# Kernel tuning notes

Hardware: AMD Instinct MI355X
Metric: run time of the kernel (lower is better)

## Reference

```python
import jax, jax.numpy as jnp
import numpy as np

WIN = (7, 7)      # window_size
SHIFT = (3, 3)    # shift_size
NUM_HEADS = 8
DIM = 256


def _relative_position_index(wh, ww):
    # static int index table, computed with numpy (constant under jit)
    coords = np.stack(np.meshgrid(np.arange(wh), np.arange(ww), indexing='ij'))  # [2,wh,ww]
    flat = coords.reshape(2, -1)                                                  # [2,N]
    rel = flat[:, :, None] - flat[:, None, :]                                     # [2,N,N]
    rel = rel.transpose(1, 2, 0).copy()
    rel[:, :, 0] += wh - 1
    rel[:, :, 1] += ww - 1
    rel[:, :, 0] *= 2 * ww - 1
    return rel.sum(-1).reshape(-1)  # [N*N]


def _attn_mask(pad_h, pad_w, win, shift):
    # static shifted-window region mask, numpy constants
    mask = np.zeros((pad_h, pad_w), dtype=np.float32)
    h_slices = ((0, -win[0]), (-win[0], -shift[0]), (-shift[0], None))
    w_slices = ((0, -win[1]), (-win[1], -shift[1]), (-shift[1], None))
    cnt = 0
    for h0, h1 in h_slices:
        for w0, w1 in w_slices:
            mask[h0:h1, w0:w1] = cnt
            cnt += 1
    nwh, nww = pad_h // win[0], pad_w // win[1]
    mask = mask.reshape(nwh, win[0], nww, win[1]).transpose(0, 2, 1, 3).reshape(nwh * nww, win[0] * win[1])
    diff = mask[:, None, :] - mask[:, :, None]
    return np.where(diff != 0, -100.0, 0.0).astype(np.float32)  # [nW, N, N]


def shifted_window_attention(x, qkv_weight, qkv_bias, proj_weight, proj_bias, rel_pos_table):
    B, H, W, C = x.shape
    wh, ww = WIN
    pad_b = (wh - H % wh) % wh
    pad_r = (ww - W % ww) % ww
    x = jnp.pad(x, ((0, 0), (0, pad_b), (0, pad_r), (0, 0)))
    pad_h, pad_w = H + pad_b, W + pad_r
    # replicate the original's shift-disable logic exactly
    sw, sh = SHIFT[0], SHIFT[1]
    if wh >= pad_h:
        sh = 0
    if ww >= pad_w:
        sw = 0
    shift = (sw, sh)
    shifted = sum(shift) > 0
    if shifted:
        x = jnp.roll(x, shift=(-shift[0], -shift[1]), axis=(1, 2))

    nwh, nww = pad_h // wh, pad_w // ww
    nW = nwh * nww
    N = wh * ww
    # window partition: [B*nW, N, C]
    xw = x.reshape(B, nwh, wh, nww, ww, C).transpose(0, 1, 3, 2, 4, 5).reshape(B * nW, N, C)

    qkv = xw @ qkv_weight.T + qkv_bias  # [B*nW, N, 3C]
    hd = C // NUM_HEADS
    qkv = qkv.reshape(B * nW, N, 3, NUM_HEADS, hd).transpose(2, 0, 3, 1, 4)  # [3, B*nW, H, N, hd]
    q, k, v = qkv[0], qkv[1], qkv[2]

    scale = hd ** (-0.5)
    attn = jnp.einsum('bhnd,bhmd->bhnm', q * scale, k)  # [B*nW, H, N, N]

    # relative position bias
    idx = _relative_position_index(wh, ww)  # static [N*N]
    bias = rel_pos_table[idx].reshape(N, N, NUM_HEADS).transpose(2, 0, 1)[None]  # [1,H,N,N]
    attn = attn + bias

    if shifted:
        mask = jnp.asarray(_attn_mask(pad_h, pad_w, WIN, shift))  # [nW, N, N]
        attn = attn.reshape(B, nW, NUM_HEADS, N, N) + mask[None, :, None, :, :]
        attn = attn.reshape(B * nW, NUM_HEADS, N, N)

    attn = jax.nn.softmax(attn, axis=-1)
    out = jnp.einsum('bhnm,bhmd->bhnd', attn, v)  # [B*nW, H, N, hd]
    out = out.transpose(0, 2, 1, 3).reshape(B * nW, N, C)
    out = out @ proj_weight.T + proj_bias

    # reverse window partition
    out = out.reshape(B, nwh, nww, wh, ww, C).transpose(0, 1, 3, 2, 4, 5).reshape(B, pad_h, pad_w, C)
    if shifted:
        out = jnp.roll(out, shift=(shift[0], shift[1]), axis=(1, 2))
    return out[:, :H, :W, :]


def setup_inputs() -> dict:
    key = jax.random.key(0)
    ks = jax.random.split(key, 6)
    return {
        'x': jax.random.normal(ks[0], (32, 56, 56, DIM), dtype=jnp.float32),
        'qkv_weight': jax.random.normal(ks[1], (3 * DIM, DIM), dtype=jnp.float32) * 0.02,
        'qkv_bias': jax.random.normal(ks[2], (3 * DIM,), dtype=jnp.float32) * 0.02,
        'proj_weight': jax.random.normal(ks[3], (DIM, DIM), dtype=jnp.float32) * 0.02,
        'proj_bias': jax.random.normal(ks[4], (DIM,), dtype=jnp.float32) * 0.02,
        'rel_pos_table': jax.random.normal(ks[5], ((2 * WIN[0] - 1) * (2 * WIN[1] - 1), NUM_HEADS), dtype=jnp.float32) * 0.02,
    }


def reference(x, qkv_weight, qkv_bias, proj_weight, proj_bias, rel_pos_table):
    return shifted_window_attention(x, qkv_weight, qkv_bias, proj_weight, proj_bias, rel_pos_table)
```

## Files before the change

### kernel.cpp

```cpp
#include <hip/hip_runtime.h>
#include <stdint.h>

typedef __attribute__((ext_vector_type(4))) float f32x4;
typedef __attribute__((ext_vector_type(8))) short bf16x8;
typedef __attribute__((ext_vector_type(8))) unsigned short u16x8;
typedef __attribute__((ext_vector_type(4))) unsigned short u16x4;

#define NPIX 100352
#define CDIM 256
#define QKVN 768
#define HWDIM 56

__device__ __forceinline__ unsigned short f2bf(float f) {
  union { float f; unsigned int u; } cv; cv.f = f;
  unsigned int u = cv.u;
  unsigned int r = (u + 0x7FFFu + ((u >> 16) & 1u)) >> 16;
  return (unsigned short)r;
}
__device__ __forceinline__ float bf2f(unsigned short h) {
  union { unsigned int u; float f; } cv; cv.u = ((unsigned int)h) << 16;
  return cv.f;
}

__global__ __launch_bounds__(256) void wqkv_pre(const float* __restrict__ w,
                                                unsigned short* __restrict__ wtab) {
  int e8 = blockIdx.x * 256 + threadIdx.x;
  int l = e8 & 63;
  int t1 = e8 >> 6;
  int wsel = t1 & 1;
  int ks = (t1 >> 1) & 7;
  int h = (t1 >> 4) & 7;
  int m = t1 >> 7;
  int row = m * 256 + h * 32 + wsel * 16 + (l & 15);
  int col = ks * 32 + (l >> 4) * 8;
  const float4* src = reinterpret_cast<const float4*>(w + (size_t)row * 256 + col);
  float4 a = src[0], b = src[1];
  u16x8 r;
  r[0] = f2bf(a.x); r[1] = f2bf(a.y); r[2] = f2bf(a.z); r[3] = f2bf(a.w);
  r[4] = f2bf(b.x); r[5] = f2bf(b.y); r[6] = f2bf(b.z); r[7] = f2bf(b.w);
  *reinterpret_cast<u16x8*>(wtab + (size_t)e8 * 8) = r;
}

__global__ __launch_bounds__(256) void wproj_pre(const float* __restrict__ w,
                                                 unsigned short* __restrict__ wptab) {
  int e8 = blockIdx.x * 256 + threadIdx.x;
  int l = e8 & 63;
  int t1 = e8 >> 6;
  int wsel = t1 & 1;
  int ks = (t1 >> 1) & 7;
  int h = (t1 >> 4) & 7;
  int row = h * 32 + wsel * 16 + (l & 15);
  int col = ks * 32 + (l >> 4) * 8;
  const float4* src = reinterpret_cast<const float4*>(w + (size_t)row * 256 + col);
  float4 a = src[0], b = src[1];
  u16x8 r;
  r[0] = f2bf(a.x); r[1] = f2bf(a.y); r[2] = f2bf(a.z); r[3] = f2bf(a.w);
  r[4] = f2bf(b.x); r[5] = f2bf(b.y); r[6] = f2bf(b.z); r[7] = f2bf(b.w);
  *reinterpret_cast<u16x8*>(wptab + (size_t)e8 * 8) = r;
}

__global__ __launch_bounds__(256) void bias_pre(const float* __restrict__ table,
                                                unsigned short* __restrict__ bt) {
  int e = blockIdx.x * 256 + threadIdx.x;
  int r  = e & 3;
  int fr = (e >> 2) & 15;
  int q  = (e >> 6) & 3;
  int c2 = (e >> 8) & 3;
  int jf = (e >> 10) & 3;
  int h  = (e >> 12) & 7;
  int cls = (e >> 15) & 3;
  int j = jf * 16 + q * 4 + r;
  int i = c2 * 16 + fr;
  float v;
  if (j > 48 || i > 48) {
    v = -1e30f;
  } else {
    int bh = cls >> 1, bw = cls & 1;
    int iwi = i / 7, iwj = i % 7;
    int jwi = j / 7, jwj = j % 7;
    int ireg = (bh ? ((iwi < 4) ? 1 : 2) : 0) * 3 + (bw ? ((iwj < 4) ? 1 : 2) : 0);
    int jreg = (bh ? ((jwi < 4) ? 1 : 2) : 0) * 3 + (bw ? ((jwj < 4) ? 1 : 2) : 0);
    float m = (ireg == jreg) ? 0.f : -100.f;
    v = table[((iwi - jwi + 6) * 13 + (iwj - jwj + 6)) * 8 + h] + m;
  }
  bt[e] = f2bf(v);
}

__global__ __launch_bounds__(512, 2) void fused_attn(
    const float* __restrict__ x,
    const unsigned short* __restrict__ wtab,
    const float* __restrict__ bqkv,
    const unsigned short* __restrict__ btab,
    const unsigned short* __restrict__ wptab,
    const float* __restrict__ bproj,
    float* __restrict__ out)
{
  const int win = blockIdx.x;
  const int b = win >> 6;
  const int gi = (win >> 3) & 7;
  const int gj = win & 7;
  const int t = threadIdx.x;
  const int head = t >> 6;
  const int lane = t & 63;
  const int fr = lane & 15;
  const int q = lane >> 4;

  __shared__ unsigned short x_s[49 * 256];
  __shared__ unsigned short Vt[8][32 * 70];
  __shared__ int pix_s[64];

  if (t < 64) {
    int idx = (t < 49) ? t : 48;
    int wi = idx / 7, wj = idx - (idx / 7) * 7;
    int hs = gi * 7 + wi, ws2 = gj * 7 + wj;
    int ph = hs + 3; if (ph >= HWDIM) ph -= HWDIM;
    int pw = ws2 + 3; if (pw >= HWDIM) pw -= HWDIM;
    pix_s[t] = (b * HWDIM + ph) * HWDIM + pw;
  }
  __syncthreads();

  #define XS(row, bc) ((unsigned)((row) * 512 + (((bc)) ^ (((row) & 7) << 4))))

  for (int u = t; u < 49 * 32; u += 512) {
    int pix = u >> 5, seg = u & 31;
    const float4* src = reinterpret_cast<const float4*>(x + (size_t)pix_s[pix] * CDIM + seg * 8);
    float4 a = src[0], c = src[1];
    u16x8 r;
    r[0] = f2bf(a.x); r[1] = f2bf(a.y); r[2] = f2bf(a.z); r[3] = f2bf(a.w);
    r[4] = f2bf(c.x); r[5] = f2bf(c.y); r[6] = f2bf(c.z); r[7] = f2bf(c.w);
    *reinterpret_cast<u16x8*>((char*)x_s + XS(pix, seg * 16)) = r;
  }
  __syncthreads();

  const int cls = (((gi == 7) ? 1 : 0) << 1) | ((gj == 7) ? 1 : 0);
  const unsigned short* bth = btab + (((cls << 3) | head) << 12);
  unsigned short* VtW = Vt[head];
  const int srcA = ((q & 1) << 5) + fr;
  const int srcB = srcA + 16;
  const bool hi = (q >= 2);

  #define PACK_MAT(pkm)                                                                \
  { _Pragma("unroll") for (int d = 0; d < 2; ++d)                                      \
      _Pragma("unroll") for (int p2 = 0; p2 < 4; ++p2) {                               \
        pkm[d][p2][0] = (unsigned)f2bf(acc[d][p2][0]) | ((unsigned)f2bf(acc[d][p2][1]) << 16); \
        pkm[d][p2][1] = (unsigned)f2bf(acc[d][p2][2]) | ((unsigned)f2bf(acc[d][p2][3]) << 16); \
      } }

  #define BUILD_FRAG(pkm, p2, dst)                                                     \
  { unsigned a0 = (unsigned)__shfl((int)pkm[0][p2][0], srcA);                          \
    unsigned a1 = (unsigned)__shfl((int)pkm[0][p2][1], srcA);                          \
    unsigned a2 = (unsigned)__shfl((int)pkm[0][p2][0], srcB);                          \
    unsigned a3 = (unsigned)__shfl((int)pkm[0][p2][1], srcB);                          \
    unsigned b0 = (unsigned)__shfl((int)pkm[1][p2][0], srcA);                          \
    unsigned b1 = (unsigned)__shfl((int)pkm[1][p2][1], srcA);                          \
    unsigned b2 = (unsigned)__shfl((int)pkm[1][p2][0], srcB);                          \
    unsigned b3 = (unsigned)__shfl((int)pkm[1][p2][1], srcB);                          \
    union { unsigned u[4]; bf16x8 v; } uf;                                             \
    uf.u[0] = hi ? b0 : a0; uf.u[1] = hi ? b1 : a1;                                    \
    uf.u[2] = hi ? b2 : a2; uf.u[3] = hi ? b3 : a3;                                    \
    dst = uf.v; }

  unsigned pkk[2][4][2], pkq[2][4][2];
  {
    f32x4 acc[2][4];
    #pragma unroll 1
    for (int m = 0; m < 3; ++m) {
      const int mat = 2 - m;
      #pragma unroll
      for (int d = 0; d < 2; ++d)
        #pragma unroll
        for (int p2 = 0; p2 < 4; ++p2)
          acc[d][p2] = (f32x4){0.f, 0.f, 0.f, 0.f};
      #pragma unroll
      for (int ks = 0; ks < 8; ++ks) {
        const unsigned short* wb = wtab + (size_t)((((mat * 8 + head) * 8 + ks) * 128 + lane) * 8);
        bf16x8 wf0 = *reinterpret_cast<const bf16x8*>(wb);
        bf16x8 wf1 = *reinterpret_cast<const bf16x8*>(wb + 512);
        int bc = ks * 64 + q * 16;
        bf16x8 xf0 = *reinterpret_cast<const bf16x8*>((const char*)x_s + XS(fr, bc));
        bf16x8 xf1 = *reinterpret_cast<const bf16x8*>((const char*)x_s + XS(16 + fr, bc));
        bf16x8 xf2 = *reinterpret_cast<const bf16x8*>((const char*)x_s + XS(32 + fr, bc));
        bf16x8 x3r = *reinterpret_cast<const bf16x8*>((const char*)x_s + XS(48, bc));
        bf16x8 xf3 = (fr == 0) ? x3r : (bf16x8){0, 0, 0, 0, 0, 0, 0, 0};
        acc[0][0] = __builtin_amdgcn_mfma_f32_16x16x32_bf16(wf0, xf0, acc[0][0], 0, 0, 0);
        acc[0][1] = __builtin_amdgcn_mfma_f32_16x16x32_bf16(wf0, xf1, acc[0][1], 0, 0, 0);
        acc[0][2] = __builtin_amdgcn_mfma_f32_16x16x32_bf16(wf0, xf2, acc[0][2], 0, 0, 0);
        acc[0][3] = __builtin_amdgcn_mfma_f32_16x16x32_bf16(wf0, xf3, acc[0][3], 0, 0, 0);
        acc[1][0] = __builtin_amdgcn_mfma_f32_16x16x32_bf16(wf1, xf0, acc[1][0], 0, 0, 0);
        acc[1][1] = __builtin_amdgcn_mfma_f32_16x16x32_bf16(wf1, xf1, acc[1][1], 0, 0, 0);
        acc[1][2] = __builtin_amdgcn_mfma_f32_16x16x32_bf16(wf1, xf2, acc[1][2], 0, 0, 0);
        acc[1][3] = __builtin_amdgcn_mfma_f32_16x16x32_bf16(wf1, xf3, acc[1][3], 0, 0, 0);
      }
      #pragma unroll
      for (int d = 0; d < 2; ++d) {
        f32x4 bv = *reinterpret_cast<const f32x4*>(bqkv + mat * 256 + head * 32 + d * 16 + q * 4);
        acc[d][0] += bv; acc[d][1] += bv; acc[d][2] += bv; acc[d][3] += bv;
      }
      if (mat == 2) {
        #pragma unroll
        for (int d = 0; d < 2; ++d)
          #pragma unroll
          for (int p2 = 0; p2 < 4; ++p2)
            #pragma unroll
            for (int r = 0; r < 4; ++r)
              VtW[(d * 16 + q * 4 + r) * 70 + p2 * 16 + fr] = f2bf(acc[d][p2][r]);
      } else if (mat == 1) {
        PACK_MAT(pkk);
      } else {
        PACK_MAT(pkq);
      }
    }
  }

  bf16x8 qf[4];
  BUILD_FRAG(pkq, 0, qf[0]); BUILD_FRAG(pkq, 1, qf[1]);
  BUILD_FRAG(pkq, 2, qf[2]); BUILD_FRAG(pkq, 3, qf[3]);

  const float scale = 0.17677669529663687f;
  u16x4 aw[2][4];
  #pragma unroll
  for (int c2 = 0; c2 < 4; ++c2)
    aw[0][c2] = *reinterpret_cast<const u16x4*>(bth + (c2 << 8) + (q << 6) + (fr << 2));
  float colsum[4] = {0.f, 0.f, 0.f, 0.f};
  unsigned pk[4][4][2];
  #pragma unroll
  for (int jf = 0; jf < 4; ++jf) {
    bf16x8 kfj;
    BUILD_FRAG(pkk, jf, kfj);
    f32x4 sacc[4];
    #pragma unroll
    for (int c2 = 0; c2 < 4; ++c2) {
      f32x4 z = {0.f, 0.f, 0.f, 0.f};
      sacc[c2] = __builtin_amdgcn_mfma_f32_16x16x32_bf16(kfj, qf[c2], z, 0, 0, 0);
    }
    if (jf < 3) {
      #pragma unroll
      for (int c2 = 0; c2 < 4; ++c2)
        aw[(jf + 1) & 1][c2] = *reinterpret_cast<const u16x4*>(
            bth + (((jf + 1) * 4 + c2) << 8) + (q << 6) + (fr << 2));
    }
    #pragma unroll
    for (int c2 = 0; c2 < 4; ++c2) {
      float ev[4];
      #pragma unroll
      for (int r = 0; r < 4; ++r) {
        float val = fmaf(sacc[c2][r], scale, bf2f(aw[jf & 1][c2][r]));
        ev[r] = __expf(val);
        colsum[c2] += ev[r];
      }
      unsigned h0 = f2bf(ev[0]), h1 = f2bf(ev[1]);
      unsigned h2 = f2bf(ev[2]), h3 = f2bf(ev[3]);
      pk[jf][c2][0] = h0 | (h1 << 16);
      pk[jf][c2][1] = h2 | (h3 << 16);
    }
  }
  float rinv[4];
  #pragma unroll
  for (int c2 = 0; c2 < 4; ++c2) {
    float s = colsum[c2];
    s += __shfl_xor(s, 16);
    s += __shfl_xor(s, 32);
    rinv[c2] = 1.0f / s;
  }

  f32x4 outT[2][4] = {};
  #pragma unroll
  for (int kb = 0; kb < 2; ++kb) {
    bf16x8 vf0 = *reinterpret_cast<const bf16x8*>(&VtW[(fr)      * 70 + kb * 32 + q * 8]);
    bf16x8 vf1 = *reinterpret_cast<const bf16x8*>(&VtW[(16 + fr) * 70 + kb * 32 + q * 8]);
    #pragma unroll
    for (int c2 = 0; c2 < 4; ++c2) {
      bf16x8 pf;
      {
        unsigned a0 = (unsigned)__shfl((int)pk[2 * kb][c2][0], srcA);
        unsigned a1 = (unsigned)__shfl((int)pk[2 * kb][c2][1], srcA);
        unsigned a2 = (unsigned)__shfl((int)pk[2 * kb][c2][0], srcB);
        unsigned a3 = (unsigned)__shfl((int)pk[2 * kb][c2][1], srcB);
        unsigned b0 = (unsigned)__shfl((int)pk[2 * kb + 1][c2][0], srcA);
        unsigned b1 = (unsigned)__shfl((int)pk[2 * kb + 1][c2][1], srcA);
        unsigned b2 = (unsigned)__shfl((int)pk[2 * kb + 1][c2][0], srcB);
        unsigned b3 = (unsigned)__shfl((int)pk[2 * kb + 1][c2][1], srcB);
        union { unsigned u[4]; bf16x8 v; } pfv;
        pfv.u[0] = hi ? b0 : a0;
        pfv.u[1] = hi ? b1 : a1;
        pfv.u[2] = hi ? b2 : a2;
        pfv.u[3] = hi ? b3 : a3;
        pf = pfv.v;
      }
      outT[0][c2] = __builtin_amdgcn_mfma_f32_16x16x32_bf16(vf0, pf, outT[0][c2], 0, 0, 0);
      outT[1][c2] = __builtin_amdgcn_mfma_f32_16x16x32_bf16(vf1, pf, outT[1][c2], 0, 0, 0);
    }
  }

  unsigned short* out_s = x_s;
  __syncthreads();
  #pragma unroll
  for (int c2 = 0; c2 < 4; ++c2) {
    int i = c2 * 16 + fr;
    if (i < 49) {
      float rv = rinv[c2];
      #pragma unroll
      for (int nt = 0; nt < 2; ++nt) {
        f32x4 o = outT[nt][c2];
        u16x4 pkd;
        pkd[0] = f2bf(o[0] * rv); pkd[1] = f2bf(o[1] * rv);
        pkd[2] = f2bf(o[2] * rv); pkd[3] = f2bf(o[3] * rv);
        *reinterpret_cast<u16x4*>((char*)out_s + XS(i, head * 64 + nt * 32 + q * 8)) = pkd;
      }
    }
  }
  __syncthreads();

  {
    f32x4 pacc[2][4];
    #pragma unroll
    for (int w = 0; w < 2; ++w)
      #pragma unroll
      for (int p2 = 0; p2 < 4; ++p2)
        pacc[w][p2] = (f32x4){0.f, 0.f, 0.f, 0.f};
    #pragma unroll
    for (int ks = 0; ks < 8; ++ks) {
      const unsigned short* wb = wptab + (size_t)((((head * 8 + ks) * 2) * 64 + lane) * 8);
      bf16x8 wp0 = *reinterpret_cast<const bf16x8*>(wb);
      bf16x8 wp1 = *reinterpret_cast<const bf16x8*>(wb + 512);
      int bc = ks * 64 + q * 16;
      bf16x8 of0 = *reinterpret_cast<const bf16x8*>((const char*)out_s + XS(fr, bc));
      bf16x8 of1 = *reinterpret_cast<const bf16x8*>((const char*)out_s + XS(16 + fr, bc));
      bf16x8 of2 = *reinterpret_cast<const bf16x8*>((const char*)out_s + XS(32 + fr, bc));
      bf16x8 o3r = *reinterpret_cast<const bf16x8*>((const char*)out_s + XS(48, bc));
      bf16x8 of3 = (fr == 0) ? o3r : (bf16x8){0, 0, 0, 0, 0, 0, 0, 0};
      pacc[0][0] = __builtin_amdgcn_mfma_f32_16x16x32_bf16(of0, wp0, pacc[0][0], 0, 0, 0);
      pacc[0][1] = __builtin_amdgcn_mfma_f32_16x16x32_bf16(of1, wp0, pacc[0][1], 0, 0, 0);
      pacc[0][2] = __builtin_amdgcn_mfma_f32_16x16x32_bf16(of2, wp0, pacc[0][2], 0, 0, 0);
      pacc[0][3] = __builtin_amdgcn_mfma_f32_16x16x32_bf16(of3, wp0, pacc[0][3], 0, 0, 0);
      pacc[1][0] = __builtin_amdgcn_mfma_f32_16x16x32_bf16(of0, wp1, pacc[1][0], 0, 0, 0);
      pacc[1][1] = __builtin_amdgcn_mfma_f32_16x16x32_bf16(of1, wp1, pacc[1][1], 0, 0, 0);
      pacc[1][2] = __builtin_amdgcn_mfma_f32_16x16x32_bf16(of2, wp1, pacc[1][2], 0, 0, 0);
      pacc[1][3] = __builtin_amdgcn_mfma_f32_16x16x32_bf16(of3, wp1, pacc[1][3], 0, 0, 0);
    }
    float bb0 = bproj[head * 32 + fr];
    float bb1 = bproj[head * 32 + 16 + fr];
    #pragma unroll
    for (int p2 = 0; p2 < 4; ++p2) {
      #pragma unroll
      for (int r = 0; r < 4; ++r) {
        int pix = p2 * 16 + q * 4 + r;
        if (pix < 49) {
          float* op = out + (size_t)pix_s[pix] * CDIM + head * 32 + fr;
          op[0]  = pacc[0][p2][r] + bb0;
          op[16] = pacc[1][p2][r] + bb1;
        }
      }
    }
  }
  #undef PACK_MAT
  #undef BUILD_FRAG
  #undef XS
}

extern "C" void kernel_launch(void* const* d_in, const int* in_sizes, int n_in,
                              void* d_out, int out_size, void* d_ws, size_t ws_size,
                              hipStream_t stream) {
  const float* x      = (const float*)d_in[0];
  const float* qkv_w  = (const float*)d_in[1];
  const float* qkv_b  = (const float*)d_in[2];
  const float* proj_w = (const float*)d_in[3];
  const float* proj_b = (const float*)d_in[4];
  const float* table  = (const float*)d_in[5];

  char* ws = (char*)d_ws;
  unsigned short* btab  = (unsigned short*)ws;
  unsigned short* wtab  = (unsigned short*)(ws + 262144);
  unsigned short* wptab = (unsigned short*)(ws + 655360);

  bias_pre<<<512, 256, 0, stream>>>(table, btab);
  wqkv_pre<<<96, 256, 0, stream>>>(qkv_w, wtab);
  wproj_pre<<<32, 256, 0, stream>>>(proj_w, wptab);

  fused_attn<<<2048, 512, 0, stream>>>(x, wtab, qkv_b, btab, wptab, proj_b,
                                       (float*)d_out);
}
```

Before: 157.3 us.

## Process four windows per persistent block and use packed bf16 conversion

Each block now loops over four consecutive windows instead of handling one, so the grid shrinks from 2048 to 512 blocks. The x-gather loop is unrolled with pixel addresses computed inline, which removes the barrier that used to follow the pix_s setup. Manual bf16 rounding is replaced with the packed __float22bfloat162_rn intrinsic. The aim is to amortise block launch and setup and to cut conversion instructions. In exchange there is an extra barrier per window and no overlap between windows inside a block, and 512 blocks at two per CU may leave CUs idle or the last wave unbalanced.

```diff
diff --git a/kernel.cpp b/kernel.cpp
--- a/kernel.cpp
+++ b/kernel.cpp
@@ -1,4 +1,5 @@
 #include <hip/hip_runtime.h>
+#include <hip/hip_bf16.h>
 #include <stdint.h>
 
 typedef __attribute__((ext_vector_type(4))) float f32x4;
@@ -20,6 +21,12 @@
 __device__ __forceinline__ float bf2f(unsigned short h) {
   union { unsigned int u; float f; } cv; cv.u = ((unsigned int)h) << 16;
   return cv.f;
+}
+__device__ __forceinline__ unsigned pk2(float lo, float hi) {
+  float2 a; a.x = lo; a.y = hi;
+  __hip_bfloat162 h = __float22bfloat162_rn(a);
+  union { __hip_bfloat162 h; unsigned u; } cv; cv.h = h;
+  return cv.u;
 }
 
 __global__ __launch_bounds__(256) void wqkv_pre(const float* __restrict__ w,
@@ -95,55 +102,30 @@
     const float* __restrict__ bproj,
     float* __restrict__ out)
 {
-  const int win = blockIdx.x;
-  const int b = win >> 6;
-  const int gi = (win >> 3) & 7;
-  const int gj = win & 7;
+  const int bid = blockIdx.x;
   const int t = threadIdx.x;
   const int head = t >> 6;
   const int lane = t & 63;
   const int fr = lane & 15;
   const int q = lane >> 4;
+  const int b = bid >> 4;
 
   __shared__ unsigned short x_s[49 * 256];
   __shared__ unsigned short Vt[8][32 * 70];
   __shared__ int pix_s[64];
 
-  if (t < 64) {
-    int idx = (t < 49) ? t : 48;
-    int wi = idx / 7, wj = idx - (idx / 7) * 7;
-    int hs = gi * 7 + wi, ws2 = gj * 7 + wj;
-    int ph = hs + 3; if (ph >= HWDIM) ph -= HWDIM;
-    int pw = ws2 + 3; if (pw >= HWDIM) pw -= HWDIM;
-    pix_s[t] = (b * HWDIM + ph) * HWDIM + pw;
-  }
-  __syncthreads();
-
-  #define XS(row, bc) ((unsigned)((row) * 512 + (((bc)) ^ (((row) & 7) << 4))))
-
-  for (int u = t; u < 49 * 32; u += 512) {
-    int pix = u >> 5, seg = u & 31;
-    const float4* src = reinterpret_cast<const float4*>(x + (size_t)pix_s[pix] * CDIM + seg * 8);
-    float4 a = src[0], c = src[1];
-    u16x8 r;
-    r[0] = f2bf(a.x); r[1] = f2bf(a.y); r[2] = f2bf(a.z); r[3] = f2bf(a.w);
-    r[4] = f2bf(c.x); r[5] = f2bf(c.y); r[6] = f2bf(c.z); r[7] = f2bf(c.w);
-    *reinterpret_cast<u16x8*>((char*)x_s + XS(pix, seg * 16)) = r;
-  }
-  __syncthreads();
-
-  const int cls = (((gi == 7) ? 1 : 0) << 1) | ((gj == 7) ? 1 : 0);
-  const unsigned short* bth = btab + (((cls << 3) | head) << 12);
-  unsigned short* VtW = Vt[head];
   const int srcA = ((q & 1) << 5) + fr;
   const int srcB = srcA + 16;
   const bool hi = (q >= 2);
+  unsigned short* VtW = Vt[head];
+
+  #define XS(row, bc) ((unsigned)((row) * 512 + (((bc)) ^ (((row) & 7) << 4))))
 
   #define PACK_MAT(pkm)                                                                \
   { _Pragma("unroll") for (int d = 0; d < 2; ++d)                                      \
       _Pragma("unroll") for (int p2 = 0; p2 < 4; ++p2) {                               \
-        pkm[d][p2][0] = (unsigned)f2bf(acc[d][p2][0]) | ((unsigned)f2bf(acc[d][p2][1]) << 16); \
-        pkm[d][p2][1] = (unsigned)f2bf(acc[d][p2][2]) | ((unsigned)f2bf(acc[d][p2][3]) << 16); \
+        pkm[d][p2][0] = pk2(acc[d][p2][0], acc[d][p2][1]);                             \
+        pkm[d][p2][1] = pk2(acc[d][p2][2], acc[d][p2][3]);                             \
       } }
 
   #define BUILD_FRAG(pkm, p2, dst)                                                     \
@@ -160,195 +142,232 @@
     uf.u[2] = hi ? b2 : a2; uf.u[3] = hi ? b3 : a3;                                    \
     dst = uf.v; }
 
-  unsigned pkk[2][4][2], pkq[2][4][2];
-  {
-    f32x4 acc[2][4];
-    #pragma unroll 1
-    for (int m = 0; m < 3; ++m) {
-      const int mat = 2 - m;
-      #pragma unroll
-      for (int d = 0; d < 2; ++d)
-        #pragma unroll
-        for (int p2 = 0; p2 < 4; ++p2)
-          acc[d][p2] = (f32x4){0.f, 0.f, 0.f, 0.f};
-      #pragma unroll
-      for (int ks = 0; ks < 8; ++ks) {
-        const unsigned short* wb = wtab + (size_t)((((mat * 8 + head) * 8 + ks) * 128 + lane) * 8);
-        bf16x8 wf0 = *reinterpret_cast<const bf16x8*>(wb);
-        bf16x8 wf1 = *reinterpret_cast<const bf16x8*>(wb + 512);
-        int bc = ks * 64 + q * 16;
-        bf16x8 xf0 = *reinterpret_cast<const bf16x8*>((const char*)x_s + XS(fr, bc));
-        bf16x8 xf1 = *reinterpret_cast<const bf16x8*>((const char*)x_s + XS(16 + fr, bc));
-        bf16x8 xf2 = *reinterpret_cast<const bf16x8*>((const char*)x_s + XS(32 + fr, bc));
-        bf16x8 x3r = *reinterpret_cast<const bf16x8*>((const char*)x_s + XS(48, bc));
-        bf16x8 xf3 = (fr == 0) ? x3r : (bf16x8){0, 0, 0, 0, 0, 0, 0, 0};
-        acc[0][0] = __builtin_amdgcn_mfma_f32_16x16x32_bf16(wf0, xf0, acc[0][0], 0, 0, 0);
-        acc[0][1] = __builtin_amdgcn_mfma_f32_16x16x32_bf16(wf0, xf1, acc[0][1], 0, 0, 0);
-        acc[0][2] = __builtin_amdgcn_mfma_f32_16x16x32_bf16(wf0, xf2, acc[0][2], 0, 0, 0);
-        acc[0][3] = __builtin_amdgcn_mfma_f32_16x16x32_bf16(wf0, xf3, acc[0][3], 0, 0, 0);
-        acc[1][0] = __builtin_amdgcn_mfma_f32_16x16x32_bf16(wf1, xf0, acc[1][0], 0, 0, 0);
-        acc[1][1] = __builtin_amdgcn_mfma_f32_16x16x32_bf16(wf1, xf1, acc[1][1], 0, 0, 0);
-        acc[1][2] = __builtin_amdgcn_mfma_f32_16x16x32_bf16(wf1, xf2, acc[1][2], 0, 0, 0);
-        acc[1][3] = __builtin_amdgcn_mfma_f32_16x16x32_bf16(wf1, xf3, acc[1][3], 0, 0, 0);
-      }
-      #pragma unroll
-      for (int d = 0; d < 2; ++d) {
-        f32x4 bv = *reinterpret_cast<const f32x4*>(bqkv + mat * 256 + head * 32 + d * 16 + q * 4);
-        acc[d][0] += bv; acc[d][1] += bv; acc[d][2] += bv; acc[d][3] += bv;
-      }
-      if (mat == 2) {
+  #pragma unroll 1
+  for (int g = 0; g < 4; ++g) {
+    const int win = (bid << 2) | g;
+    const int gi = (win >> 3) & 7;
+    const int gj = win & 7;
+
+    if (g) __syncthreads();
+
+    if (t < 64) {
+      int idx = (t < 49) ? t : 48;
+      int wi = idx / 7, wj = idx - (idx / 7) * 7;
+      int ph = gi * 7 + wi + 3; if (ph >= HWDIM) ph -= HWDIM;
+      int pw = gj * 7 + wj + 3; if (pw >= HWDIM) pw -= HWDIM;
+      pix_s[t] = (b * HWDIM + ph) * HWDIM + pw;
+    }
+
+    #pragma unroll
+    for (int k = 0; k < 4; ++k) {
+      int u = t + 512 * k;
+      if (u < 1568) {
+        int pix = u >> 5, seg = u & 31;
+        int wi = pix / 7, wj = pix - (pix / 7) * 7;
+        int ph = gi * 7 + wi + 3; if (ph >= HWDIM) ph -= HWDIM;
+        int pw = gj * 7 + wj + 3; if (pw >= HWDIM) pw -= HWDIM;
+        int pabs = (b * HWDIM + ph) * HWDIM + pw;
+        const float4* src = reinterpret_cast<const float4*>(x + (size_t)pabs * CDIM + seg * 8);
+        float4 a = src[0], c = src[1];
+        union { unsigned w[4]; u16x8 v; } r;
+        r.w[0] = pk2(a.x, a.y); r.w[1] = pk2(a.z, a.w);
+        r.w[2] = pk2(c.x, c.y); r.w[3] = pk2(c.z, c.w);
+        *reinterpret_cast<u16x8*>((char*)x_s + XS(pix, seg * 16)) = r.v;
+      }
+    }
+    __syncthreads();
+
+    const int cls = (((gi == 7) ? 1 : 0) << 1) | ((gj == 7) ? 1 : 0);
+    const unsigned short* bth = btab + (((cls << 3) | head) << 12);
+
+    unsigned pkk[2][4][2], pkq[2][4][2];
+    {
+      f32x4 acc[2][4];
+      #pragma unroll 1
+      for (int m = 0; m < 3; ++m) {
+        const int mat = 2 - m;
         #pragma unroll
         for (int d = 0; d < 2; ++d)
           #pragma unroll
           for (int p2 = 0; p2 < 4; ++p2)
+            acc[d][p2] = (f32x4){0.f, 0.f, 0.f, 0.f};
+        #pragma unroll
+        for (int ks = 0; ks < 8; ++ks) {
+          const unsigned short* wb = wtab + (size_t)((((mat * 8 + head) * 8 + ks) * 128 + lane) * 8);
+          bf16x8 wf0 = *reinterpret_cast<const bf16x8*>(wb);
+          bf16x8 wf1 = *reinterpret_cast<const bf16x8*>(wb + 512);
+          int bc = ks * 64 + q * 16;
+          bf16x8 xf0 = *reinterpret_cast<const bf16x8*>((const char*)x_s + XS(fr, bc));
+          bf16x8 xf1 = *reinterpret_cast<const bf16x8*>((const char*)x_s + XS(16 + fr, bc));
+          bf16x8 xf2 = *reinterpret_cast<const bf16x8*>((const char*)x_s + XS(32 + fr, bc));
+          bf16x8 x3r = *reinterpret_cast<const bf16x8*>((const char*)x_s + XS(48, bc));
+          bf16x8 xf3 = (fr == 0) ? x3r : (bf16x8){0, 0, 0, 0, 0, 0, 0, 0};
+          acc[0][0] = __builtin_amdgcn_mfma_f32_16x16x32_bf16(wf0, xf0, acc[0][0], 0, 0, 0);
+          acc[0][1] = __builtin_amdgcn_mfma_f32_16x16x32_bf16(wf0, xf1, acc[0][1], 0, 0, 0);
+          acc[0][2] = __builtin_amdgcn_mfma_f32_16x16x32_bf16(wf0, xf2, acc[0][2], 0, 0, 0);
+          acc[0][3] = __builtin_amdgcn_mfma_f32_16x16x32_bf16(wf0, xf3, acc[0][3], 0, 0, 0);
+          acc[1][0] = __builtin_amdgcn_mfma_f32_16x16x32_bf16(wf1, xf0, acc[1][0], 0, 0, 0);
+          acc[1][1] = __builtin_amdgcn_mfma_f32_16x16x32_bf16(wf1, xf1, acc[1][1], 0, 0, 0);
+          acc[1][2] = __builtin_amdgcn_mfma_f32_16x16x32_bf16(wf1, xf2, acc[1][2], 0, 0, 0);
+          acc[1][3] = __builtin_amdgcn_mfma_f32_16x16x32_bf16(wf1, xf3, acc[1][3], 0, 0, 0);
+        }
+        #pragma unroll
+        for (int d = 0; d < 2; ++d) {
+          f32x4 bv = *reinterpret_cast<const f32x4*>(bqkv + mat * 256 + head * 32 + d * 16 + q * 4);
+          acc[d][0] += bv; acc[d][1] += bv; acc[d][2] += bv; acc[d][3] += bv;
+        }
+        if (mat == 2) {
+          #pragma unroll
+          for (int d = 0; d < 2; ++d)
             #pragma unroll
-            for (int r = 0; r < 4; ++r)
-              VtW[(d * 16 + q * 4 + r) * 70 + p2 * 16 + fr] = f2bf(acc[d][p2][r]);
-      } else if (mat == 1) {
-        PACK_MAT(pkk);
-      } else {
-        PACK_MAT(pkq);
-      }
-    }
-  }
-
-  bf16x8 qf[4];
-  BUILD_FRAG(pkq, 0, qf[0]); BUILD_FRAG(pkq, 1, qf[1]);
-  BUILD_FRAG(pkq, 2, qf[2]); BUILD_FRAG(pkq, 3, qf[3]);
-
-  const float scale = 0.17677669529663687f;
-  u16x4 aw[2][4];
-  #pragma unroll
-  for (int c2 = 0; c2 < 4; ++c2)
-    aw[0][c2] = *reinterpret_cast<const u16x4*>(bth + (c2 << 8) + (q << 6) + (fr << 2));
-  float colsum[4] = {0.f, 0.f, 0.f, 0.f};
-  unsigned pk[4][4][2];
-  #pragma unroll
-  for (int jf = 0; jf < 4; ++jf) {
-    bf16x8 kfj;
-    BUILD_FRAG(pkk, jf, kfj);
-    f32x4 sacc[4];
+            for (int p2 = 0; p2 < 4; ++p2)
+              #pragma unroll
+              for (int r = 0; r < 4; ++r)
+                VtW[(d * 16 + q * 4 + r) * 70 + p2 * 16 + fr] = f2bf(acc[d][p2][r]);
+        } else if (mat == 1) {
+          PACK_MAT(pkk);
+        } else {
+          PACK_MAT(pkq);
+        }
+      }
+    }
+
+    bf16x8 qf[4];
+    BUILD_FRAG(pkq, 0, qf[0]); BUILD_FRAG(pkq, 1, qf[1]);
+    BUILD_FRAG(pkq, 2, qf[2]); BUILD_FRAG(pkq, 3, qf[3]);
+
+    const float scale = 0.17677669529663687f;
+    u16x4 aw[2][4];
+    #pragma unroll
+    for (int c2 = 0; c2 < 4; ++c2)
+      aw[0][c2] = *reinterpret_cast<const u16x4*>(bth + (c2 << 8) + (q << 6) + (fr << 2));
+    float colsum[4] = {0.f, 0.f, 0.f, 0.f};
+    unsigned pk[4][4][2];
+    #pragma unroll
+    for (int jf = 0; jf < 4; ++jf) {
+      bf16x8 kfj;
+      BUILD_FRAG(pkk, jf, kfj);
+      f32x4 sacc[4];
+      #pragma unroll
+      for (int c2 = 0; c2 < 4; ++c2) {
+        f32x4 z = {0.f, 0.f, 0.f, 0.f};
+        sacc[c2] = __builtin_amdgcn_mfma_f32_16x16x32_bf16(kfj, qf[c2], z, 0, 0, 0);
+      }
+      if (jf < 3) {
+        #pragma unroll
+        for (int c2 = 0; c2 < 4; ++c2)
+          aw[(jf + 1) & 1][c2] = *reinterpret_cast<const u16x4*>(
+              bth + (((jf + 1) * 4 + c2) << 8) + (q << 6) + (fr << 2));
+      }
+      #pragma unroll
+      for (int c2 = 0; c2 < 4; ++c2) {
+        float ev[4];
+        #pragma unroll
+        for (int r = 0; r < 4; ++r) {
+          float val = fmaf(sacc[c2][r], scale, bf2f(aw[jf & 1][c2][r]));
+          ev[r] = __expf(val);
+          colsum[c2] += ev[r];
+        }
+        pk[jf][c2][0] = pk2(ev[0], ev[1]);
+        pk[jf][c2][1] = pk2(ev[2], ev[3]);
+      }
+    }
+    float rinv[4];
     #pragma unroll
     for (int c2 = 0; c2 < 4; ++c2) {
-      f32x4 z = {0.f, 0.f, 0.f, 0.f};
-      sacc[c2] = __builtin_amdgcn_mfma_f32_16x16x32_bf16(kfj, qf[c2], z, 0, 0, 0);
-    }
-    if (jf < 3) {
-      #pragma unroll
-      for (int c2 = 0; c2 < 4; ++c2)
-        aw[(jf + 1) & 1][c2] = *reinterpret_cast<const u16x4*>(
-            bth + (((jf + 1) * 4 + c2) << 8) + (q << 6) + (fr << 2));
-    }
+      float s = colsum[c2];
+      s += __shfl_xor(s, 16);
+      s += __shfl_xor(s, 32);
+      rinv[c2] = 1.0f / s;
+    }
+
+    f32x4 outT[2][4] = {};
+    #pragma unroll
+    for (int kb = 0; kb < 2; ++kb) {
+      bf16x8 vf0 = *reinterpret_cast<const bf16x8*>(&VtW[(fr)      * 70 + kb * 32 + q * 8]);
+      bf16x8 vf1 = *reinterpret_cast<const bf16x8*>(&VtW[(16 + fr) * 70 + kb * 32 + q * 8]);
+      #pragma unroll
+      for (int c2 = 0; c2 < 4; ++c2) {
+        bf16x8 pf;
+        {
+          unsigned a0 = (unsigned)__shfl((int)pk[2 * kb][c2][0], srcA);
+          unsigned a1 = (unsigned)__shfl((int)pk[2 * kb][c2][1], srcA);
+          unsigned a2 = (unsigned)__shfl((int)pk[2 * kb][c2][0], srcB);
+          unsigned a3 = (unsigned)__shfl((int)pk[2 * kb][c2][1], srcB);
+          unsigned b0 = (unsigned)__shfl((int)pk[2 * kb + 1][c2][0], srcA);
+          unsigned b1 = (unsigned)__shfl((int)pk[2 * kb + 1][c2][1], srcA);
+          unsigned b2 = (unsigned)__shfl((int)pk[2 * kb + 1][c2][0], srcB);
+          unsigned b3 = (unsigned)__shfl((int)pk[2 * kb + 1][c2][1], srcB);
+          union { unsigned u[4]; bf16x8 v; } pfv;
+          pfv.u[0] = hi ? b0 : a0;
+          pfv.u[1] = hi ? b1 : a1;
+          pfv.u[2] = hi ? b2 : a2;
+          pfv.u[3] = hi ? b3 : a3;
+          pf = pfv.v;
+        }
+        outT[0][c2] = __builtin_amdgcn_mfma_f32_16x16x32_bf16(vf0, pf, outT[0][c2], 0, 0, 0);
+        outT[1][c2] = __builtin_amdgcn_mfma_f32_16x16x32_bf16(vf1, pf, outT[1][c2], 0, 0, 0);
+      }
+    }
+
+    unsigned short* out_s = x_s;
+    __syncthreads();
     #pragma unroll
     for (int c2 = 0; c2 < 4; ++c2) {
-      float ev[4];
-      #pragma unroll
-      for (int r = 0; r < 4; ++r) {
-        float val = fmaf(sacc[c2][r], scale, bf2f(aw[jf & 1][c2][r]));
-        ev[r] = __expf(val);
-        colsum[c2] += ev[r];
-      }
-      unsigned h0 = f2bf(ev[0]), h1 = f2bf(ev[1]);
-      unsigned h2 = f2bf(ev[2]), h3 = f2bf(ev[3]);
-      pk[jf][c2][0] = h0 | (h1 << 16);
-      pk[jf][c2][1] = h2 | (h3 << 16);
-    }
-  }
-  float rinv[4];
-  #pragma unroll
-  for (int c2 = 0; c2 < 4; ++c2) {
-    float s = colsum[c2];
-    s += __shfl_xor(s, 16);
-    s += __shfl_xor(s, 32);
-    rinv[c2] = 1.0f / s;
-  }
-
-  f32x4 outT[2][4] = {};
-  #pragma unroll
-  for (int kb = 0; kb < 2; ++kb) {
-    bf16x8 vf0 = *reinterpret_cast<const bf16x8*>(&VtW[(fr)      * 70 + kb * 32 + q * 8]);
-    bf16x8 vf1 = *reinterpret_cast<const bf16x8*>(&VtW[(16 + fr) * 70 + kb * 32 + q * 8]);
-    #pragma unroll
-    for (int c2 = 0; c2 < 4; ++c2) {
-      bf16x8 pf;
-      {
-        unsigned a0 = (unsigned)__shfl((int)pk[2 * kb][c2][0], srcA);
-        unsigned a1 = (unsigned)__shfl((int)pk[2 * kb][c2][1], srcA);
-        unsigned a2 = (unsigned)__shfl((int)pk[2 * kb][c2][0], srcB);
-        unsigned a3 = (unsigned)__shfl((int)pk[2 * kb][c2][1], srcB);
-        unsigned b0 = (unsigned)__shfl((int)pk[2 * kb + 1][c2][0], srcA);
-        unsigned b1 = (unsigned)__shfl((int)pk[2 * kb + 1][c2][1], srcA);
-        unsigned b2 = (unsigned)__shfl((int)pk[2 * kb + 1][c2][0], srcB);
-        unsigned b3 = (unsigned)__shfl((int)pk[2 * kb + 1][c2][1], srcB);
-        union { unsigned u[4]; bf16x8 v; } pfv;
-        pfv.u[0] = hi ? b0 : a0;
-        pfv.u[1] = hi ? b1 : a1;
-        pfv.u[2] = hi ? b2 : a2;
-        pfv.u[3] = hi ? b3 : a3;
-        pf = pfv.v;
-      }
-      outT[0][c2] = __builtin_amdgcn_mfma_f32_16x16x32_bf16(vf0, pf, outT[0][c2], 0, 0, 0);
-      outT[1][c2] = __builtin_amdgcn_mfma_f32_16x16x32_bf16(vf1, pf, outT[1][c2], 0, 0, 0);
-    }
-  }
-
-  unsigned short* out_s = x_s;
-  __syncthreads();
-  #pragma unroll
-  for (int c2 = 0; c2 < 4; ++c2) {
-    int i = c2 * 16 + fr;
-    if (i < 49) {
-      float rv = rinv[c2];
-      #pragma unroll
-      for (int nt = 0; nt < 2; ++nt) {
-        f32x4 o = outT[nt][c2];
-        u16x4 pkd;
-        pkd[0] = f2bf(o[0] * rv); pkd[1] = f2bf(o[1] * rv);
-        pkd[2] = f2bf(o[2] * rv); pkd[3] = f2bf(o[3] * rv);
-        *reinterpret_cast<u16x4*>((char*)out_s + XS(i, head * 64 + nt * 32 + q * 8)) = pkd;
-      }
-    }
-  }
-  __syncthreads();
-
-  {
-    f32x4 pacc[2][4];
-    #pragma unroll
-    for (int w = 0; w < 2; ++w)
-      #pragma unroll
-      for (int p2 = 0; p2 < 4; ++p2)
-        pacc[w][p2] = (f32x4){0.f, 0.f, 0.f, 0.f};
-    #pragma unroll
-    for (int ks = 0; ks < 8; ++ks) {
-      const unsigned short* wb = wptab + (size_t)((((head * 8 + ks) * 2) * 64 + lane) * 8);
-      bf16x8 wp0 = *reinterpret_cast<const bf16x8*>(wb);
-      bf16x8 wp1 = *reinterpret_cast<const bf16x8*>(wb + 512);
-      int bc = ks * 64 + q * 16;
-      bf16x8 of0 = *reinterpret_cast<const bf16x8*>((const char*)out_s + XS(fr, bc));
-      bf16x8 of1 = *reinterpret_cast<const bf16x8*>((const char*)out_s + XS(16 + fr, bc));
-      bf16x8 of2 = *reinterpret_cast<const bf16x8*>((const char*)out_s + XS(32 + fr, bc));
-      bf16x8 o3r = *reinterpret_cast<const bf16x8*>((const char*)out_s + XS(48, bc));
-      bf16x8 of3 = (fr == 0) ? o3r : (bf16x8){0, 0, 0, 0, 0, 0, 0, 0};
-      pacc[0][0] = __builtin_amdgcn_mfma_f32_16x16x32_bf16(of0, wp0, pacc[0][0], 0, 0, 0);
-      pacc[0][1] = __builtin_amdgcn_mfma_f32_16x16x32_bf16(of1, wp0, pacc[0][1], 0, 0, 0);
-      pacc[0][2] = __builtin_amdgcn_mfma_f32_16x16x32_bf16(of2, wp0, pacc[0][2], 0, 0, 0);
-      pacc[0][3] = __builtin_amdgcn_mfma_f32_16x16x32_bf16(of3, wp0, pacc[0][3], 0, 0, 0);
-      pacc[1][0] = __builtin_amdgcn_mfma_f32_16x16x32_bf16(of0, wp1, pacc[1][0], 0, 0, 0);
-      pacc[1][1] = __builtin_amdgcn_mfma_f32_16x16x32_bf16(of1, wp1, pacc[1][1], 0, 0, 0);
-      pacc[1][2] = __builtin_amdgcn_mfma_f32_16x16x32_bf16(of2, wp1, pacc[1][2], 0, 0, 0);
-      pacc[1][3] = __builtin_amdgcn_mfma_f32_16x16x32_bf16(of3, wp1, pacc[1][3], 0, 0, 0);
-    }
-    float bb0 = bproj[head * 32 + fr];
-    float bb1 = bproj[head * 32 + 16 + fr];
-    #pragma unroll
-    for (int p2 = 0; p2 < 4; ++p2) {
-      #pragma unroll
-      for (int r = 0; r < 4; ++r) {
-        int pix = p2 * 16 + q * 4 + r;
-        if (pix < 49) {
-          float* op = out + (size_t)pix_s[pix] * CDIM + head * 32 + fr;
-          op[0]  = pacc[0][p2][r] + bb0;
-          op[16] = pacc[1][p2][r] + bb1;
+      int i = c2 * 16 + fr;
+      if (i < 49) {
+        float rv = rinv[c2];
+        #pragma unroll
+        for (int nt = 0; nt < 2; ++nt) {
+          f32x4 o = outT[nt][c2];
+          union { unsigned w[2]; u16x4 v; } pd;
+          pd.w[0] = pk2(o[0] * rv, o[1] * rv);
+          pd.w[1] = pk2(o[2] * rv, o[3] * rv);
+          *reinterpret_cast<u16x4*>((char*)out_s + XS(i, head * 64 + nt * 32 + q * 8)) = pd.v;
+        }
+      }
+    }
+    __syncthreads();
+
+    {
+      f32x4 pacc[2][4];
+      #pragma unroll
+      for (int w = 0; w < 2; ++w)
+        #pragma unroll
+        for (int p2 = 0; p2 < 4; ++p2)
+          pacc[w][p2] = (f32x4){0.f, 0.f, 0.f, 0.f};
+      #pragma unroll
+      for (int ks = 0; ks < 8; ++ks) {
+        const unsigned short* wb = wptab + (size_t)((((head * 8 + ks) * 2) * 64 + lane) * 8);
+        bf16x8 wp0 = *reinterpret_cast<const bf16x8*>(wb);
+        bf16x8 wp1 = *reinterpret_cast<const bf16x8*>(wb + 512);
+        int bc = ks * 64 + q * 16;
+        bf16x8 of0 = *reinterpret_cast<const bf16x8*>((const char*)out_s + XS(fr, bc));
+        bf16x8 of1 = *reinterpret_cast<const bf16x8*>((const char*)out_s + XS(16 + fr, bc));
+        bf16x8 of2 = *reinterpret_cast<const bf16x8*>((const char*)out_s + XS(32 + fr, bc));
+        bf16x8 o3r = *reinterpret_cast<const bf16x8*>((const char*)out_s + XS(48, bc));
+        bf16x8 of3 = (fr == 0) ? o3r : (bf16x8){0, 0, 0, 0, 0, 0, 0, 0};
+        pacc[0][0] = __builtin_amdgcn_mfma_f32_16x16x32_bf16(of0, wp0, pacc[0][0], 0, 0, 0);
+        pacc[0][1] = __builtin_amdgcn_mfma_f32_16x16x32_bf16(of1, wp0, pacc[0][1], 0, 0, 0);
+        pacc[0][2] = __builtin_amdgcn_mfma_f32_16x16x32_bf16(of2, wp0, pacc[0][2], 0, 0, 0);
+        pacc[0][3] = __builtin_amdgcn_mfma_f32_16x16x32_bf16(of3, wp0, pacc[0][3], 0, 0, 0);
+        pacc[1][0] = __builtin_amdgcn_mfma_f32_16x16x32_bf16(of0, wp1, pacc[1][0], 0, 0, 0);
+        pacc[1][1] = __builtin_amdgcn_mfma_f32_16x16x32_bf16(of1, wp1, pacc[1][1], 0, 0, 0);
+        pacc[1][2] = __builtin_amdgcn_mfma_f32_16x16x32_bf16(of2, wp1, pacc[1][2], 0, 0, 0);
+        pacc[1][3] = __builtin_amdgcn_mfma_f32_16x16x32_bf16(of3, wp1, pacc[1][3], 0, 0, 0);
+      }
+      float bb0 = bproj[head * 32 + fr];
+      float bb1 = bproj[head * 32 + 16 + fr];
+      #pragma unroll
+      for (int p2 = 0; p2 < 4; ++p2) {
+        #pragma unroll
+        for (int r = 0; r < 4; ++r) {
+          int pix = p2 * 16 + q * 4 + r;
+          if (pix < 49) {
+            float* op = out + (size_t)pix_s[pix] * CDIM + head * 32 + fr;
+            op[0]  = pacc[0][p2][r] + bb0;
+            op[16] = pacc[1][p2][r] + bb1;
+          }
         }
       }
     }
@@ -377,6 +396,6 @@
   wqkv_pre<<<96, 256, 0, stream>>>(qkv_w, wtab);
   wproj_pre<<<32, 256, 0, stream>>>(proj_w, wptab);
 
-  fused_attn<<<2048, 512, 0, stream>>>(x, wtab, qkv_b, btab, wptab, proj_b,
-                                       (float*)d_out);
-}
+  fused_attn<<<512, 512, 0, stream>>>(x, wtab, qkv_b, btab, wptab, proj_b,
+                                      (float*)d_out);
+}
```

Result: slower. 215.0 us (+36.7%).
